# Kernel optimization log

Measured on AMD Instinct MI355X. Metric: run time of the kernel, lower is better.

The kernel has to match this reference:

```python
import jax, jax.numpy as jnp
import numpy as np

H = 1024
V = 32000
L = 4096


def setup_inputs() -> dict:
    key = jax.random.key(0)
    ks = jax.random.split(key, 20)
    s = 1.0 / np.sqrt(H)
    d = {}
    d["input_token"] = jax.random.randint(ks[0], (1,), 0, V)
    d["hidden"] = jax.random.normal(ks[1], (1, 1, H), jnp.float32)
    d["encoder_hiddens"] = jax.random.normal(ks[2], (L, H), jnp.float32)
    # parameters
    d["emb"] = jax.random.normal(ks[3], (V, H), jnp.float32)
    d["wW"] = jax.random.uniform(ks[4], (H, H), jnp.float32, -s, s)
    d["wb"] = jax.random.uniform(ks[5], (H,), jnp.float32, -s, s)
    d["uW"] = jax.random.uniform(ks[6], (H, H), jnp.float32, -s, s)
    d["ub"] = jax.random.uniform(ks[7], (H,), jnp.float32, -s, s)
    d["vW"] = jax.random.uniform(ks[8], (1, H), jnp.float32, -s, s)
    d["cW"] = jax.random.uniform(ks[9], (H, 2 * H), jnp.float32, -s, s)
    d["cb"] = jax.random.uniform(ks[10], (H,), jnp.float32, -s, s)
    d["w_ih"] = jax.random.uniform(ks[11], (3 * H, H), jnp.float32, -s, s)
    d["b_ih"] = jax.random.uniform(ks[12], (3 * H,), jnp.float32, -s, s)
    d["w_hh"] = jax.random.uniform(ks[13], (3 * H, H), jnp.float32, -s, s)
    d["b_hh"] = jax.random.uniform(ks[14], (3 * H,), jnp.float32, -s, s)
    d["outW"] = jax.random.uniform(ks[15], (V, H), jnp.float32, -s, s)
    d["outb"] = jax.random.uniform(ks[16], (V,), jnp.float32, -s, s)
    return d


def reference(input_token, hidden, encoder_hiddens, emb, wW, wb, uW, ub, vW,
              cW, cb, w_ih, b_ih, w_hh, b_hh, outW, outb):
    # embedding lookup, dropout is identity (p=0 / eval)
    embedded = emb[input_token[0]]  # [H]
    # additive attention: w(hidden[0]) + u(enc) -> tanh -> v -> softmax
    h0 = hidden[0]  # [1, H] (first/only layer)
    scores = jnp.tanh(h0 @ wW.T + wb + encoder_hiddens @ uW.T + ub) @ vW[0]  # [L]
    attn_weights = jax.nn.softmax(scores, axis=-1)  # [L]
    context = attn_weights @ encoder_hiddens  # [H]
    # combine + relu
    x = jnp.concatenate([context, embedded])  # [2H]
    x = jax.nn.relu(x @ cW.T + cb)  # [H]
    # single GRU cell step (torch GRU gate order: r, z, n)
    hprev = hidden[0, 0]  # [H]
    gi = x @ w_ih.T + b_ih
    gh = hprev @ w_hh.T + b_hh
    ir, iz, inn = jnp.split(gi, 3)
    hr, hz, hn = jnp.split(gh, 3)
    r = jax.nn.sigmoid(ir + hr)
    z = jax.nn.sigmoid(iz + hz)
    n = jnp.tanh(inn + r * hn)
    hnew = (1.0 - z) * n + z * hprev  # [H]
    new_hidden = hnew.reshape(1, 1, H)
    # residual + output projection
    out = (context.reshape(1, 1, H) + new_hidden)
    logits = out @ outW.T + outb  # [1, 1, V]
    return logits, new_hidden, attn_weights
```

## Files before the change

kernel.cpp:

```cpp
#include <hip/hip_runtime.h>
#include <hip/hip_bf16.h>
#include <math.h>

#define H 1024
#define V 32000
#define L 4096

typedef __bf16 bf16x8 __attribute__((ext_vector_type(8)));
typedef float f32x4 __attribute__((ext_vector_type(4)));

__device__ __forceinline__ unsigned short f32_to_bf16(float f) {
    unsigned int u = __float_as_uint(f);
    unsigned int r = (u + 0x7fffu + ((u >> 16) & 1u)) >> 16;
    return (unsigned short)r;
}

__device__ __forceinline__ float bf16_to_f32(unsigned short s) {
    return __uint_as_float(((unsigned int)s) << 16);
}

__device__ __forceinline__ float dot4(float4 a, float4 b) {
    return a.x * b.x + a.y * b.y + a.z * b.z + a.w * b.w;
}

__device__ __forceinline__ float wave_reduce(float v) {
    for (int off = 32; off; off >>= 1) v += __shfl_xor(v, off);
    return v;
}

__global__ __launch_bounds__(256) void prep_wh_kernel(
        const float* __restrict__ enc,
        const float* __restrict__ uW,
        const float* __restrict__ emb,
        const int* __restrict__ token,
        const float* __restrict__ h0,
        const float* __restrict__ wW,
        const float* __restrict__ wb,
        const float* __restrict__ ub,
        unsigned short* __restrict__ enc_bf,
        unsigned short* __restrict__ u_bf,
        float* __restrict__ emb_vec,
        float* __restrict__ wh,
        float* __restrict__ scores) {
    if (blockIdx.x < 1024) {
        int tid = blockIdx.x * 256 + threadIdx.x;
        const int stride = 1024 * 256;
        const int NE = L * H / 4;
        const int NU = H * H / 4;
        for (int i = tid; i < NE; i += stride) {
            float4 f = ((const float4*)enc)[i];
            ushort4 o;
            o.x = f32_to_bf16(f.x); o.y = f32_to_bf16(f.y);
            o.z = f32_to_bf16(f.z); o.w = f32_to_bf16(f.w);
            ((ushort4*)enc_bf)[i] = o;
        }
        for (int i = tid; i < NU; i += stride) {
            float4 f = ((const float4*)uW)[i];
            ushort4 o;
            o.x = f32_to_bf16(f.x); o.y = f32_to_bf16(f.y);
            o.z = f32_to_bf16(f.z); o.w = f32_to_bf16(f.w);
            ((ushort4*)u_bf)[i] = o;
        }
        int t0 = token[0];
        for (int i = tid; i < H; i += stride) emb_vec[i] = emb[(size_t)t0 * H + i];
    } else {
        int z = (blockIdx.x - 1024) * 256 + threadIdx.x;
        if (z < L) scores[z] = 0.f;
        int wave = ((blockIdx.x - 1024) * 256 + threadIdx.x) >> 6;
        int lane = threadIdx.x & 63;
        const float4* row = (const float4*)(wW + (size_t)wave * H);
        const float4* hv = (const float4*)h0;
        float acc = 0.f;
#pragma unroll
        for (int i = 0; i < 4; i++) {
            int idx = i * 64 + lane;
            acc += dot4(row[idx], hv[idx]);
        }
        acc = wave_reduce(acc);
        if (lane == 0) wh[wave] = acc + wb[wave] + ub[wave];
    }
}

#define APITCH 72
__global__ __launch_bounds__(256) void scores_kernel(
        const unsigned short* __restrict__ enc_bf,
        const unsigned short* __restrict__ u_bf,
        const float* __restrict__ wh,
        const float* __restrict__ vW,
        float* __restrict__ scores,
        float* __restrict__ context) {
    __shared__ unsigned short Als[64 * APITCH];
    __shared__ unsigned short Bls[128 * APITCH];
    int tid = threadIdx.x;
    if (blockIdx.x == 0 && blockIdx.y == 0) {
        ((float4*)context)[tid] = make_float4(0.f, 0.f, 0.f, 0.f);
    }
    int wave = tid >> 6, lane = tid & 63;
    int wm = wave >> 1, wn = wave & 1;
    int mrow = lane & 15, quad = lane >> 4;
    int r0b = blockIdx.x * 64;
    int jc0b = blockIdx.y * 128;

    f32x4 acc[2][4];
#pragma unroll
    for (int mt = 0; mt < 2; mt++)
#pragma unroll
        for (int jt = 0; jt < 4; jt++) acc[mt][jt] = (f32x4){0.f, 0.f, 0.f, 0.f};

    for (int k0 = 0; k0 < H; k0 += 64) {
#pragma unroll
        for (int c = 0; c < 2; c++) {
            int chunk = c * 256 + tid;
            int row = chunk >> 3, ko = (chunk & 7) * 8;
            *(uint4*)(Als + row * APITCH + ko) =
                *(const uint4*)(enc_bf + (size_t)(r0b + row) * H + k0 + ko);
        }
#pragma unroll
        for (int c = 0; c < 4; c++) {
            int chunk = c * 256 + tid;
            int j = chunk >> 3, ko = (chunk & 7) * 8;
            *(uint4*)(Bls + j * APITCH + ko) =
                *(const uint4*)(u_bf + (size_t)(jc0b + j) * H + k0 + ko);
        }
        __syncthreads();

        bf16x8 a[2][2];
#pragma unroll
        for (int mt = 0; mt < 2; mt++) {
            const unsigned short* abase =
                Als + (wm * 32 + mt * 16 + mrow) * APITCH + quad * 8;
            a[mt][0] = *(const bf16x8*)(abase);
            a[mt][1] = *(const bf16x8*)(abase + 32);
        }
#pragma unroll
        for (int jt = 0; jt < 4; jt++) {
            const unsigned short* bbase =
                Bls + (wn * 64 + jt * 16 + mrow) * APITCH + quad * 8;
            bf16x8 b0 = *(const bf16x8*)(bbase);
            bf16x8 b1 = *(const bf16x8*)(bbase + 32);
#pragma unroll
            for (int mt = 0; mt < 2; mt++) {
                acc[mt][jt] = __builtin_amdgcn_mfma_f32_16x16x32_bf16(a[mt][0], b0, acc[mt][jt], 0, 0, 0);
                acc[mt][jt] = __builtin_amdgcn_mfma_f32_16x16x32_bf16(a[mt][1], b1, acc[mt][jt], 0, 0, 0);
            }
        }
        __syncthreads();
    }

    float sacc[2][4] = {{0.f, 0.f, 0.f, 0.f}, {0.f, 0.f, 0.f, 0.f}};
#pragma unroll
    for (int jt = 0; jt < 4; jt++) {
        int jcol = jc0b + wn * 64 + jt * 16 + mrow;
        float vj = vW[jcol];
        float whv = wh[jcol];
#pragma unroll
        for (int mt = 0; mt < 2; mt++)
#pragma unroll
            for (int r = 0; r < 4; r++)
                sacc[mt][r] += vj * tanhf(acc[mt][jt][r] + whv);
    }
#pragma unroll
    for (int mt = 0; mt < 2; mt++)
#pragma unroll
        for (int r = 0; r < 4; r++) {
            float s = sacc[mt][r];
            s += __shfl_xor(s, 1);
            s += __shfl_xor(s, 2);
            s += __shfl_xor(s, 4);
            s += __shfl_xor(s, 8);
            if (mrow == 0)
                atomicAdd(&scores[r0b + wm * 32 + mt * 16 + quad * 4 + r], s);
        }
}

__global__ __launch_bounds__(256) void ctx_softmax_kernel(
        const float* __restrict__ scores,
        const unsigned short* __restrict__ enc_bf,
        float* __restrict__ context,
        float* __restrict__ attn_out) {
    __shared__ float smax[4];
    __shared__ float ssum[4];
    __shared__ float attn_l[32];
    int tid = threadIdx.x;
    int wid = tid >> 6, lane = tid & 63;
    float4 s0 = ((const float4*)scores)[tid];
    float4 s1 = ((const float4*)scores)[256 + tid];
    float4 s2 = ((const float4*)scores)[512 + tid];
    float4 s3 = ((const float4*)scores)[768 + tid];
    float m = fmaxf(fmaxf(fmaxf(s0.x, s0.y), fmaxf(s0.z, s0.w)),
                    fmaxf(fmaxf(s1.x, s1.y), fmaxf(s1.z, s1.w)));
    m = fmaxf(m, fmaxf(fmaxf(s2.x, s2.y), fmaxf(s2.z, s2.w)));
    m = fmaxf(m, fmaxf(fmaxf(s3.x, s3.y), fmaxf(s3.z, s3.w)));
    for (int off = 32; off; off >>= 1) m = fmaxf(m, __shfl_xor(m, off));
    if (lane == 0) smax[wid] = m;
    __syncthreads();
    float gmax = fmaxf(fmaxf(smax[0], smax[1]), fmaxf(smax[2], smax[3]));
    float e = expf(s0.x - gmax) + expf(s0.y - gmax) + expf(s0.z - gmax) + expf(s0.w - gmax)
            + expf(s1.x - gmax) + expf(s1.y - gmax) + expf(s1.z - gmax) + expf(s1.w - gmax)
            + expf(s2.x - gmax) + expf(s2.y - gmax) + expf(s2.z - gmax) + expf(s2.w - gmax)
            + expf(s3.x - gmax) + expf(s3.y - gmax) + expf(s3.z - gmax) + expf(s3.w - gmax);
    e = wave_reduce(e);
    if (lane == 0) ssum[wid] = e;
    __syncthreads();
    float inv = 1.0f / (ssum[0] + ssum[1] + ssum[2] + ssum[3]);

    int l0 = blockIdx.y * 32;
    if (tid < 32) attn_l[tid] = expf(scores[l0 + tid] - gmax) * inv;
    __syncthreads();

    if (blockIdx.x == 0 && blockIdx.y == 0) {
        float4 a0 = make_float4(expf(s0.x - gmax) * inv, expf(s0.y - gmax) * inv,
                                expf(s0.z - gmax) * inv, expf(s0.w - gmax) * inv);
        float4 a1 = make_float4(expf(s1.x - gmax) * inv, expf(s1.y - gmax) * inv,
                                expf(s1.z - gmax) * inv, expf(s1.w - gmax) * inv);
        float4 a2 = make_float4(expf(s2.x - gmax) * inv, expf(s2.y - gmax) * inv,
                                expf(s2.z - gmax) * inv, expf(s2.w - gmax) * inv);
        float4 a3 = make_float4(expf(s3.x - gmax) * inv, expf(s3.y - gmax) * inv,
                                expf(s3.z - gmax) * inv, expf(s3.w - gmax) * inv);
        ((float4*)attn_out)[tid] = a0;
        ((float4*)attn_out)[256 + tid] = a1;
        ((float4*)attn_out)[512 + tid] = a2;
        ((float4*)attn_out)[768 + tid] = a3;
    }

    int col = blockIdx.x * 256 + tid;
    float acc = 0.f;
#pragma unroll 4
    for (int l = 0; l < 32; l++)
        acc += attn_l[l] * bf16_to_f32(enc_bf[(size_t)(l0 + l) * H + col]);
    atomicAdd(&context[col], acc);
}

__global__ void combine_kernel(const float* __restrict__ context,
                               const float* __restrict__ emb_vec,
                               const float* __restrict__ cW,
                               const float* __restrict__ cb,
                               float* __restrict__ xvec) {
    int wave = (blockIdx.x * blockDim.x + threadIdx.x) >> 6;
    int lane = threadIdx.x & 63;
    if (wave >= H) return;
    const float4* row = (const float4*)(cW + (size_t)wave * 2 * H);
    const float4* cv = (const float4*)context;
    const float4* ev = (const float4*)emb_vec;
    float acc = 0.f;
#pragma unroll
    for (int i = 0; i < 4; i++) {
        int idx = i * 64 + lane;
        acc += dot4(row[idx], cv[idx]);
        acc += dot4(row[256 + idx], ev[idx]);
    }
    acc = wave_reduce(acc);
    if (lane == 0) xvec[wave] = fmaxf(acc + cb[wave], 0.f);
}

__global__ void gru_kernel(const float* __restrict__ xvec,
                           const float* __restrict__ hprev,
                           const float* __restrict__ w_ih,
                           const float* __restrict__ b_ih,
                           const float* __restrict__ w_hh,
                           const float* __restrict__ b_hh,
                           const float* __restrict__ context,
                           float* __restrict__ hnew_out,
                           float* __restrict__ ovec) {
    int j = (blockIdx.x * blockDim.x + threadIdx.x) >> 6;
    int lane = threadIdx.x & 63;
    if (j >= H) return;
    const float4* xv = (const float4*)xvec;
    const float4* hv = (const float4*)hprev;
    float a0 = 0.f, a1 = 0.f, a2 = 0.f, a3 = 0.f, a4 = 0.f, a5 = 0.f;
#pragma unroll
    for (int i = 0; i < 4; i++) {
        int idx = i * 64 + lane;
        float4 x4 = xv[idx], h4 = hv[idx];
        a0 += dot4(((const float4*)(w_ih + (size_t)j * H))[idx], x4);
        a1 += dot4(((const float4*)(w_ih + (size_t)(H + j) * H))[idx], x4);
        a2 += dot4(((const float4*)(w_ih + (size_t)(2 * H + j) * H))[idx], x4);
        a3 += dot4(((const float4*)(w_hh + (size_t)j * H))[idx], h4);
        a4 += dot4(((const float4*)(w_hh + (size_t)(H + j) * H))[idx], h4);
        a5 += dot4(((const float4*)(w_hh + (size_t)(2 * H + j) * H))[idx], h4);
    }
    a0 = wave_reduce(a0); a1 = wave_reduce(a1); a2 = wave_reduce(a2);
    a3 = wave_reduce(a3); a4 = wave_reduce(a4); a5 = wave_reduce(a5);
    if (lane == 0) {
        float ir = a0 + b_ih[j], iz = a1 + b_ih[H + j], inn = a2 + b_ih[2 * H + j];
        float hr = a3 + b_hh[j], hz = a4 + b_hh[H + j], hn = a5 + b_hh[2 * H + j];
        float r = 1.f / (1.f + expf(-(ir + hr)));
        float z = 1.f / (1.f + expf(-(iz + hz)));
        float n = tanhf(inn + r * hn);
        float hp = hprev[j];
        float hval = (1.f - z) * n + z * hp;
        hnew_out[j] = hval;
        ovec[j] = context[j] + hval;
    }
}

__global__ __launch_bounds__(256) void logits_kernel(
        const float* __restrict__ ovec,
        const float* __restrict__ outW,
        const float* __restrict__ outb,
        float* __restrict__ out) {
    int wave = (blockIdx.x * blockDim.x + threadIdx.x) >> 6;
    int lane = threadIdx.x & 63;
    int i0 = wave * 2;
    if (i0 >= V) return;
    const float4* row0 = (const float4*)(outW + (size_t)i0 * H);
    const float4* row1 = (const float4*)(outW + (size_t)(i0 + 1) * H);
    const float4* ov = (const float4*)ovec;
    float acc0 = 0.f, acc1 = 0.f;
#pragma unroll
    for (int t = 0; t < 4; t++) {
        int idx = t * 64 + lane;
        float4 o4 = ov[idx];
        acc0 += dot4(row0[idx], o4);
        acc1 += dot4(row1[idx], o4);
    }
    acc0 = wave_reduce(acc0);
    acc1 = wave_reduce(acc1);
    if (lane == 0) {
        out[i0] = acc0 + outb[i0];
        out[i0 + 1] = acc1 + outb[i0 + 1];
    }
}

extern "C" void kernel_launch(void* const* d_in, const int* in_sizes, int n_in,
                              void* d_out, int out_size, void* d_ws, size_t ws_size,
                              hipStream_t stream) {
    const int* token = (const int*)d_in[0];
    const float* hidden = (const float*)d_in[1];
    const float* enc = (const float*)d_in[2];
    const float* emb = (const float*)d_in[3];
    const float* wW = (const float*)d_in[4];
    const float* wb = (const float*)d_in[5];
    const float* uW = (const float*)d_in[6];
    const float* ub = (const float*)d_in[7];
    const float* vW = (const float*)d_in[8];
    const float* cW = (const float*)d_in[9];
    const float* cb = (const float*)d_in[10];
    const float* w_ih = (const float*)d_in[11];
    const float* b_ih = (const float*)d_in[12];
    const float* w_hh = (const float*)d_in[13];
    const float* b_hh = (const float*)d_in[14];
    const float* outW = (const float*)d_in[15];
    const float* outb = (const float*)d_in[16];
    float* out = (float*)d_out;

    char* ws = (char*)d_ws;
    unsigned short* enc_bf = (unsigned short*)ws;
    unsigned short* u_bf = (unsigned short*)(ws + (size_t)L * H * 2);
    float* whv = (float*)(ws + (size_t)L * H * 2 + (size_t)H * H * 2);
    float* emb_vec = whv + H;
    float* scores = emb_vec + H;
    float* context = scores + L;
    float* xvec = context + H;
    float* ovec = xvec + H;

    prep_wh_kernel<<<1280, 256, 0, stream>>>(enc, uW, emb, token, hidden, wW, wb, ub,
                                             enc_bf, u_bf, emb_vec, whv, scores);
    scores_kernel<<<dim3(64, 8), 256, 0, stream>>>(enc_bf, u_bf, whv, vW, scores, context);
    ctx_softmax_kernel<<<dim3(4, 128), 256, 0, stream>>>(scores, enc_bf, context, out + V + H);
    combine_kernel<<<256, 256, 0, stream>>>(context, emb_vec, cW, cb, xvec);
    gru_kernel<<<256, 256, 0, stream>>>(xvec, hidden, w_ih, b_ih, w_hh, b_hh,
                                        context, out + V, ovec);
    logits_kernel<<<4000, 256, 0, stream>>>(ovec, outW, outb, out);
}
```

Before: 338.7 us.

## Fuse all stages into one persistent kernel with software grid barriers

Replaces six separate launches with a single persistent kernel of 256 blocks that separates stages with an atomic-counter grid barrier. The hidden-to-hidden GRU matvec is hoisted into the first stage alongside the bf16 conversion. The attention GEMM tile is enlarged and the logits stage loops over rows per wave. This removes launch gaps and inter-kernel idle time, at the risk of barrier spin cost, reduced parallelism in the memory-bound phases, and a timeout fallback that could break correctness if blocks are not co-resident.

```diff
diff --git a/kernel.cpp b/kernel.cpp
--- a/kernel.cpp
+++ b/kernel.cpp
@@ -1,10 +1,12 @@
 #include <hip/hip_runtime.h>
-#include <hip/hip_bf16.h>
 #include <math.h>
 
 #define H 1024
 #define V 32000
 #define L 4096
+#define NBLK 256
+#define NTHR 512
+#define APITCH 72
 
 typedef __bf16 bf16x8 __attribute__((ext_vector_type(8)));
 typedef float f32x4 __attribute__((ext_vector_type(4)));
@@ -28,297 +30,317 @@
     return v;
 }
 
-__global__ __launch_bounds__(256) void prep_wh_kernel(
+__device__ __forceinline__ void grid_sync(unsigned* bar) {
+    __threadfence();
+    __syncthreads();
+    if (threadIdx.x == 0) {
+        unsigned g = __hip_atomic_load(&bar[1], __ATOMIC_RELAXED, __HIP_MEMORY_SCOPE_AGENT);
+        unsigned a = __hip_atomic_fetch_add(&bar[0], 1u, __ATOMIC_ACQ_REL, __HIP_MEMORY_SCOPE_AGENT);
+        if (a == NBLK - 1u) {
+            __hip_atomic_store(&bar[0], 0u, __ATOMIC_RELAXED, __HIP_MEMORY_SCOPE_AGENT);
+            __hip_atomic_store(&bar[1], g + 1u, __ATOMIC_RELEASE, __HIP_MEMORY_SCOPE_AGENT);
+        } else {
+            unsigned long long t0 = __builtin_amdgcn_s_memrealtime();
+            while (__hip_atomic_load(&bar[1], __ATOMIC_ACQUIRE, __HIP_MEMORY_SCOPE_AGENT) == g) {
+                __builtin_amdgcn_s_sleep(4);
+                if (__builtin_amdgcn_s_memrealtime() - t0 > 500000ull) break;
+            }
+        }
+    }
+    __syncthreads();
+    __threadfence();
+}
+
+__global__ __launch_bounds__(NTHR, 2) void mega_kernel(
+        const int* __restrict__ token,
+        const float* __restrict__ hidden,
         const float* __restrict__ enc,
-        const float* __restrict__ uW,
         const float* __restrict__ emb,
-        const int* __restrict__ token,
-        const float* __restrict__ h0,
         const float* __restrict__ wW,
         const float* __restrict__ wb,
+        const float* __restrict__ uW,
         const float* __restrict__ ub,
+        const float* __restrict__ vW,
+        const float* __restrict__ cW,
+        const float* __restrict__ cb,
+        const float* __restrict__ w_ih,
+        const float* __restrict__ b_ih,
+        const float* __restrict__ w_hh,
+        const float* __restrict__ b_hh,
+        const float* __restrict__ outW,
+        const float* __restrict__ outb,
+        float* __restrict__ out,
+        unsigned* __restrict__ bar,
+        float* __restrict__ wh,
+        float* __restrict__ gh,
+        float* __restrict__ scores,
+        float* __restrict__ context,
+        float* __restrict__ xvec,
+        float* __restrict__ ovec,
         unsigned short* __restrict__ enc_bf,
-        unsigned short* __restrict__ u_bf,
-        float* __restrict__ emb_vec,
-        float* __restrict__ wh,
-        float* __restrict__ scores) {
-    if (blockIdx.x < 1024) {
-        int tid = blockIdx.x * 256 + threadIdx.x;
-        const int stride = 1024 * 256;
+        unsigned short* __restrict__ u_bf) {
+    __shared__ unsigned short Als[128 * APITCH];
+    __shared__ unsigned short Bls[128 * APITCH];
+    __shared__ float smax[8];
+    __shared__ float ssum[8];
+    __shared__ float attn_l[32];
+
+    const int tid = threadIdx.x;
+    const int blk = blockIdx.x;
+    const int gt = blk * NTHR + tid;
+    const int wid = tid >> 6, lane = tid & 63;
+    const int gw = gt >> 6;
+
+    {
+        const int GSZ = NBLK * NTHR;
         const int NE = L * H / 4;
-        const int NU = H * H / 4;
-        for (int i = tid; i < NE; i += stride) {
+        for (int i = gt; i < NE; i += GSZ) {
             float4 f = ((const float4*)enc)[i];
             ushort4 o;
             o.x = f32_to_bf16(f.x); o.y = f32_to_bf16(f.y);
             o.z = f32_to_bf16(f.z); o.w = f32_to_bf16(f.w);
             ((ushort4*)enc_bf)[i] = o;
         }
-        for (int i = tid; i < NU; i += stride) {
+        const int NU = H * H / 4;
+        for (int i = gt; i < NU; i += GSZ) {
             float4 f = ((const float4*)uW)[i];
             ushort4 o;
             o.x = f32_to_bf16(f.x); o.y = f32_to_bf16(f.y);
             o.z = f32_to_bf16(f.z); o.w = f32_to_bf16(f.w);
             ((ushort4*)u_bf)[i] = o;
         }
-        int t0 = token[0];
-        for (int i = tid; i < H; i += stride) emb_vec[i] = emb[(size_t)t0 * H + i];
-    } else {
-        int z = (blockIdx.x - 1024) * 256 + threadIdx.x;
-        if (z < L) scores[z] = 0.f;
-        int wave = ((blockIdx.x - 1024) * 256 + threadIdx.x) >> 6;
-        int lane = threadIdx.x & 63;
-        const float4* row = (const float4*)(wW + (size_t)wave * H);
-        const float4* hv = (const float4*)h0;
+        if (gt < L / 4) ((float4*)scores)[gt] = make_float4(0.f, 0.f, 0.f, 0.f);
+        else if (gt < L / 4 + H / 4)
+            ((float4*)context)[gt - L / 4] = make_float4(0.f, 0.f, 0.f, 0.f);
+        if (gw < H) {
+            const float4* row = (const float4*)(wW + (size_t)gw * H);
+            const float4* hv = (const float4*)hidden;
+            float acc = 0.f;
+#pragma unroll
+            for (int i = 0; i < 4; i++) {
+                int idx = i * 64 + lane;
+                acc += dot4(row[idx], hv[idx]);
+            }
+            acc = wave_reduce(acc);
+            if (lane == 0) wh[gw] = acc + wb[gw] + ub[gw];
+        } else {
+            int j = gw - H;
+            const float4* hv = (const float4*)hidden;
+            float a3 = 0.f, a4 = 0.f, a5 = 0.f;
+#pragma unroll
+            for (int i = 0; i < 4; i++) {
+                int idx = i * 64 + lane;
+                float4 h4 = hv[idx];
+                a3 += dot4(((const float4*)(w_hh + (size_t)j * H))[idx], h4);
+                a4 += dot4(((const float4*)(w_hh + (size_t)(H + j) * H))[idx], h4);
+                a5 += dot4(((const float4*)(w_hh + (size_t)(2 * H + j) * H))[idx], h4);
+            }
+            a3 = wave_reduce(a3); a4 = wave_reduce(a4); a5 = wave_reduce(a5);
+            if (lane == 0) {
+                gh[j] = a3 + b_hh[j];
+                gh[H + j] = a4 + b_hh[H + j];
+                gh[2 * H + j] = a5 + b_hh[2 * H + j];
+            }
+        }
+    }
+    grid_sync(bar);
+
+    {
+        const int bx = blk & 31, by = blk >> 5;
+        const int r0b = bx * 128, jc0b = by * 128;
+        const int wm = wid >> 1, wn = wid & 1;
+        const int mrow = lane & 15, quad = lane >> 4;
+
+        f32x4 acc[2][4];
+#pragma unroll
+        for (int mt = 0; mt < 2; mt++)
+#pragma unroll
+            for (int jt = 0; jt < 4; jt++) acc[mt][jt] = (f32x4){0.f, 0.f, 0.f, 0.f};
+
+        for (int k0 = 0; k0 < H; k0 += 64) {
+#pragma unroll
+            for (int c = 0; c < 2; c++) {
+                int chunk = c * NTHR + tid;
+                int row = chunk >> 3, ko = (chunk & 7) * 8;
+                *(uint4*)(Als + row * APITCH + ko) =
+                    *(const uint4*)(enc_bf + (size_t)(r0b + row) * H + k0 + ko);
+            }
+#pragma unroll
+            for (int c = 0; c < 2; c++) {
+                int chunk = c * NTHR + tid;
+                int j = chunk >> 3, ko = (chunk & 7) * 8;
+                *(uint4*)(Bls + j * APITCH + ko) =
+                    *(const uint4*)(u_bf + (size_t)(jc0b + j) * H + k0 + ko);
+            }
+            __syncthreads();
+
+            bf16x8 a[2][2];
+#pragma unroll
+            for (int mt = 0; mt < 2; mt++) {
+                const unsigned short* abase =
+                    Als + (wm * 32 + mt * 16 + mrow) * APITCH + quad * 8;
+                a[mt][0] = *(const bf16x8*)(abase);
+                a[mt][1] = *(const bf16x8*)(abase + 32);
+            }
+#pragma unroll
+            for (int jt = 0; jt < 4; jt++) {
+                const unsigned short* bbase =
+                    Bls + (wn * 64 + jt * 16 + mrow) * APITCH + quad * 8;
+                bf16x8 b0 = *(const bf16x8*)(bbase);
+                bf16x8 b1 = *(const bf16x8*)(bbase + 32);
+#pragma unroll
+                for (int mt = 0; mt < 2; mt++) {
+                    acc[mt][jt] = __builtin_amdgcn_mfma_f32_16x16x32_bf16(a[mt][0], b0, acc[mt][jt], 0, 0, 0);
+                    acc[mt][jt] = __builtin_amdgcn_mfma_f32_16x16x32_bf16(a[mt][1], b1, acc[mt][jt], 0, 0, 0);
+                }
+            }
+            __syncthreads();
+        }
+
+        float sacc[2][4] = {{0.f, 0.f, 0.f, 0.f}, {0.f, 0.f, 0.f, 0.f}};
+#pragma unroll
+        for (int jt = 0; jt < 4; jt++) {
+            int jcol = jc0b + wn * 64 + jt * 16 + mrow;
+            float vj = vW[jcol];
+            float whv = wh[jcol];
+#pragma unroll
+            for (int mt = 0; mt < 2; mt++)
+#pragma unroll
+                for (int r = 0; r < 4; r++)
+                    sacc[mt][r] += vj * tanhf(acc[mt][jt][r] + whv);
+        }
+#pragma unroll
+        for (int mt = 0; mt < 2; mt++)
+#pragma unroll
+            for (int r = 0; r < 4; r++) {
+                float s = sacc[mt][r];
+                s += __shfl_xor(s, 1);
+                s += __shfl_xor(s, 2);
+                s += __shfl_xor(s, 4);
+                s += __shfl_xor(s, 8);
+                if (mrow == 0)
+                    atomicAdd(&scores[r0b + wm * 32 + mt * 16 + quad * 4 + r], s);
+            }
+    }
+    grid_sync(bar);
+
+    {
+        const int cx = blk & 1, ly = blk >> 1;
+        float4 s0 = ((const float4*)scores)[tid];
+        float4 s1 = ((const float4*)scores)[512 + tid];
+        float m = fmaxf(fmaxf(fmaxf(s0.x, s0.y), fmaxf(s0.z, s0.w)),
+                        fmaxf(fmaxf(s1.x, s1.y), fmaxf(s1.z, s1.w)));
+        for (int off = 32; off; off >>= 1) m = fmaxf(m, __shfl_xor(m, off));
+        if (lane == 0) smax[wid] = m;
+        __syncthreads();
+        float gmax = smax[0];
+#pragma unroll
+        for (int w = 1; w < 8; w++) gmax = fmaxf(gmax, smax[w]);
+        float e = expf(s0.x - gmax) + expf(s0.y - gmax) + expf(s0.z - gmax) + expf(s0.w - gmax)
+                + expf(s1.x - gmax) + expf(s1.y - gmax) + expf(s1.z - gmax) + expf(s1.w - gmax);
+        e = wave_reduce(e);
+        if (lane == 0) ssum[wid] = e;
+        __syncthreads();
+        float tot = ssum[0];
+#pragma unroll
+        for (int w = 1; w < 8; w++) tot += ssum[w];
+        float inv = 1.0f / tot;
+
+        int l0 = ly * 32;
+        if (tid < 32) attn_l[tid] = expf(scores[l0 + tid] - gmax) * inv;
+        __syncthreads();
+
+        if (blk == 0) {
+            float* attn_out = out + V + H;
+            float4 a0 = make_float4(expf(s0.x - gmax) * inv, expf(s0.y - gmax) * inv,
+                                    expf(s0.z - gmax) * inv, expf(s0.w - gmax) * inv);
+            float4 a1 = make_float4(expf(s1.x - gmax) * inv, expf(s1.y - gmax) * inv,
+                                    expf(s1.z - gmax) * inv, expf(s1.w - gmax) * inv);
+            ((float4*)attn_out)[tid] = a0;
+            ((float4*)attn_out)[512 + tid] = a1;
+        }
+
+        int col = cx * 512 + tid;
         float acc = 0.f;
-#pragma unroll
-        for (int i = 0; i < 4; i++) {
-            int idx = i * 64 + lane;
-            acc += dot4(row[idx], hv[idx]);
-        }
-        acc = wave_reduce(acc);
-        if (lane == 0) wh[wave] = acc + wb[wave] + ub[wave];
-    }
-}
-
-#define APITCH 72
-__global__ __launch_bounds__(256) void scores_kernel(
-        const unsigned short* __restrict__ enc_bf,
-        const unsigned short* __restrict__ u_bf,
-        const float* __restrict__ wh,
-        const float* __restrict__ vW,
-        float* __restrict__ scores,
-        float* __restrict__ context) {
-    __shared__ unsigned short Als[64 * APITCH];
-    __shared__ unsigned short Bls[128 * APITCH];
-    int tid = threadIdx.x;
-    if (blockIdx.x == 0 && blockIdx.y == 0) {
-        ((float4*)context)[tid] = make_float4(0.f, 0.f, 0.f, 0.f);
-    }
-    int wave = tid >> 6, lane = tid & 63;
-    int wm = wave >> 1, wn = wave & 1;
-    int mrow = lane & 15, quad = lane >> 4;
-    int r0b = blockIdx.x * 64;
-    int jc0b = blockIdx.y * 128;
-
-    f32x4 acc[2][4];
-#pragma unroll
-    for (int mt = 0; mt < 2; mt++)
-#pragma unroll
-        for (int jt = 0; jt < 4; jt++) acc[mt][jt] = (f32x4){0.f, 0.f, 0.f, 0.f};
-
-    for (int k0 = 0; k0 < H; k0 += 64) {
-#pragma unroll
-        for (int c = 0; c < 2; c++) {
-            int chunk = c * 256 + tid;
-            int row = chunk >> 3, ko = (chunk & 7) * 8;
-            *(uint4*)(Als + row * APITCH + ko) =
-                *(const uint4*)(enc_bf + (size_t)(r0b + row) * H + k0 + ko);
-        }
-#pragma unroll
-        for (int c = 0; c < 4; c++) {
-            int chunk = c * 256 + tid;
-            int j = chunk >> 3, ko = (chunk & 7) * 8;
-            *(uint4*)(Bls + j * APITCH + ko) =
-                *(const uint4*)(u_bf + (size_t)(jc0b + j) * H + k0 + ko);
-        }
-        __syncthreads();
-
-        bf16x8 a[2][2];
-#pragma unroll
-        for (int mt = 0; mt < 2; mt++) {
-            const unsigned short* abase =
-                Als + (wm * 32 + mt * 16 + mrow) * APITCH + quad * 8;
-            a[mt][0] = *(const bf16x8*)(abase);
-            a[mt][1] = *(const bf16x8*)(abase + 32);
-        }
-#pragma unroll
-        for (int jt = 0; jt < 4; jt++) {
-            const unsigned short* bbase =
-                Bls + (wn * 64 + jt * 16 + mrow) * APITCH + quad * 8;
-            bf16x8 b0 = *(const bf16x8*)(bbase);
-            bf16x8 b1 = *(const bf16x8*)(bbase + 32);
-#pragma unroll
-            for (int mt = 0; mt < 2; mt++) {
-                acc[mt][jt] = __builtin_amdgcn_mfma_f32_16x16x32_bf16(a[mt][0], b0, acc[mt][jt], 0, 0, 0);
-                acc[mt][jt] = __builtin_amdgcn_mfma_f32_16x16x32_bf16(a[mt][1], b1, acc[mt][jt], 0, 0, 0);
-            }
-        }
-        __syncthreads();
-    }
-
-    float sacc[2][4] = {{0.f, 0.f, 0.f, 0.f}, {0.f, 0.f, 0.f, 0.f}};
-#pragma unroll
-    for (int jt = 0; jt < 4; jt++) {
-        int jcol = jc0b + wn * 64 + jt * 16 + mrow;
-        float vj = vW[jcol];
-        float whv = wh[jcol];
-#pragma unroll
-        for (int mt = 0; mt < 2; mt++)
-#pragma unroll
-            for (int r = 0; r < 4; r++)
-                sacc[mt][r] += vj * tanhf(acc[mt][jt][r] + whv);
-    }
-#pragma unroll
-    for (int mt = 0; mt < 2; mt++)
-#pragma unroll
-        for (int r = 0; r < 4; r++) {
-            float s = sacc[mt][r];
-            s += __shfl_xor(s, 1);
-            s += __shfl_xor(s, 2);
-            s += __shfl_xor(s, 4);
-            s += __shfl_xor(s, 8);
-            if (mrow == 0)
-                atomicAdd(&scores[r0b + wm * 32 + mt * 16 + quad * 4 + r], s);
-        }
-}
-
-__global__ __launch_bounds__(256) void ctx_softmax_kernel(
-        const float* __restrict__ scores,
-        const unsigned short* __restrict__ enc_bf,
-        float* __restrict__ context,
-        float* __restrict__ attn_out) {
-    __shared__ float smax[4];
-    __shared__ float ssum[4];
-    __shared__ float attn_l[32];
-    int tid = threadIdx.x;
-    int wid = tid >> 6, lane = tid & 63;
-    float4 s0 = ((const float4*)scores)[tid];
-    float4 s1 = ((const float4*)scores)[256 + tid];
-    float4 s2 = ((const float4*)scores)[512 + tid];
-    float4 s3 = ((const float4*)scores)[768 + tid];
-    float m = fmaxf(fmaxf(fmaxf(s0.x, s0.y), fmaxf(s0.z, s0.w)),
-                    fmaxf(fmaxf(s1.x, s1.y), fmaxf(s1.z, s1.w)));
-    m = fmaxf(m, fmaxf(fmaxf(s2.x, s2.y), fmaxf(s2.z, s2.w)));
-    m = fmaxf(m, fmaxf(fmaxf(s3.x, s3.y), fmaxf(s3.z, s3.w)));
-    for (int off = 32; off; off >>= 1) m = fmaxf(m, __shfl_xor(m, off));
-    if (lane == 0) smax[wid] = m;
-    __syncthreads();
-    float gmax = fmaxf(fmaxf(smax[0], smax[1]), fmaxf(smax[2], smax[3]));
-    float e = expf(s0.x - gmax) + expf(s0.y - gmax) + expf(s0.z - gmax) + expf(s0.w - gmax)
-            + expf(s1.x - gmax) + expf(s1.y - gmax) + expf(s1.z - gmax) + expf(s1.w - gmax)
-            + expf(s2.x - gmax) + expf(s2.y - gmax) + expf(s2.z - gmax) + expf(s2.w - gmax)
-            + expf(s3.x - gmax) + expf(s3.y - gmax) + expf(s3.z - gmax) + expf(s3.w - gmax);
-    e = wave_reduce(e);
-    if (lane == 0) ssum[wid] = e;
-    __syncthreads();
-    float inv = 1.0f / (ssum[0] + ssum[1] + ssum[2] + ssum[3]);
-
-    int l0 = blockIdx.y * 32;
-    if (tid < 32) attn_l[tid] = expf(scores[l0 + tid] - gmax) * inv;
-    __syncthreads();
-
-    if (blockIdx.x == 0 && blockIdx.y == 0) {
-        float4 a0 = make_float4(expf(s0.x - gmax) * inv, expf(s0.y - gmax) * inv,
-                                expf(s0.z - gmax) * inv, expf(s0.w - gmax) * inv);
-        float4 a1 = make_float4(expf(s1.x - gmax) * inv, expf(s1.y - gmax) * inv,
-                                expf(s1.z - gmax) * inv, expf(s1.w - gmax) * inv);
-        float4 a2 = make_float4(expf(s2.x - gmax) * inv, expf(s2.y - gmax) * inv,
-                                expf(s2.z - gmax) * inv, expf(s2.w - gmax) * inv);
-        float4 a3 = make_float4(expf(s3.x - gmax) * inv, expf(s3.y - gmax) * inv,
-                                expf(s3.z - gmax) * inv, expf(s3.w - gmax) * inv);
-        ((float4*)attn_out)[tid] = a0;
-        ((float4*)attn_out)[256 + tid] = a1;
-        ((float4*)attn_out)[512 + tid] = a2;
-        ((float4*)attn_out)[768 + tid] = a3;
-    }
-
-    int col = blockIdx.x * 256 + tid;
-    float acc = 0.f;
 #pragma unroll 4
-    for (int l = 0; l < 32; l++)
-        acc += attn_l[l] * bf16_to_f32(enc_bf[(size_t)(l0 + l) * H + col]);
-    atomicAdd(&context[col], acc);
-}
-
-__global__ void combine_kernel(const float* __restrict__ context,
-                               const float* __restrict__ emb_vec,
-                               const float* __restrict__ cW,
-                               const float* __restrict__ cb,
-                               float* __restrict__ xvec) {
-    int wave = (blockIdx.x * blockDim.x + threadIdx.x) >> 6;
-    int lane = threadIdx.x & 63;
-    if (wave >= H) return;
-    const float4* row = (const float4*)(cW + (size_t)wave * 2 * H);
-    const float4* cv = (const float4*)context;
-    const float4* ev = (const float4*)emb_vec;
-    float acc = 0.f;
-#pragma unroll
-    for (int i = 0; i < 4; i++) {
-        int idx = i * 64 + lane;
-        acc += dot4(row[idx], cv[idx]);
-        acc += dot4(row[256 + idx], ev[idx]);
-    }
-    acc = wave_reduce(acc);
-    if (lane == 0) xvec[wave] = fmaxf(acc + cb[wave], 0.f);
-}
-
-__global__ void gru_kernel(const float* __restrict__ xvec,
-                           const float* __restrict__ hprev,
-                           const float* __restrict__ w_ih,
-                           const float* __restrict__ b_ih,
-                           const float* __restrict__ w_hh,
-                           const float* __restrict__ b_hh,
-                           const float* __restrict__ context,
-                           float* __restrict__ hnew_out,
-                           float* __restrict__ ovec) {
-    int j = (blockIdx.x * blockDim.x + threadIdx.x) >> 6;
-    int lane = threadIdx.x & 63;
-    if (j >= H) return;
-    const float4* xv = (const float4*)xvec;
-    const float4* hv = (const float4*)hprev;
-    float a0 = 0.f, a1 = 0.f, a2 = 0.f, a3 = 0.f, a4 = 0.f, a5 = 0.f;
-#pragma unroll
-    for (int i = 0; i < 4; i++) {
-        int idx = i * 64 + lane;
-        float4 x4 = xv[idx], h4 = hv[idx];
-        a0 += dot4(((const float4*)(w_ih + (size_t)j * H))[idx], x4);
-        a1 += dot4(((const float4*)(w_ih + (size_t)(H + j) * H))[idx], x4);
-        a2 += dot4(((const float4*)(w_ih + (size_t)(2 * H + j) * H))[idx], x4);
-        a3 += dot4(((const float4*)(w_hh + (size_t)j * H))[idx], h4);
-        a4 += dot4(((const float4*)(w_hh + (size_t)(H + j) * H))[idx], h4);
-        a5 += dot4(((const float4*)(w_hh + (size_t)(2 * H + j) * H))[idx], h4);
-    }
-    a0 = wave_reduce(a0); a1 = wave_reduce(a1); a2 = wave_reduce(a2);
-    a3 = wave_reduce(a3); a4 = wave_reduce(a4); a5 = wave_reduce(a5);
-    if (lane == 0) {
-        float ir = a0 + b_ih[j], iz = a1 + b_ih[H + j], inn = a2 + b_ih[2 * H + j];
-        float hr = a3 + b_hh[j], hz = a4 + b_hh[H + j], hn = a5 + b_hh[2 * H + j];
-        float r = 1.f / (1.f + expf(-(ir + hr)));
-        float z = 1.f / (1.f + expf(-(iz + hz)));
-        float n = tanhf(inn + r * hn);
-        float hp = hprev[j];
-        float hval = (1.f - z) * n + z * hp;
-        hnew_out[j] = hval;
-        ovec[j] = context[j] + hval;
-    }
-}
-
-__global__ __launch_bounds__(256) void logits_kernel(
-        const float* __restrict__ ovec,
-        const float* __restrict__ outW,
-        const float* __restrict__ outb,
-        float* __restrict__ out) {
-    int wave = (blockIdx.x * blockDim.x + threadIdx.x) >> 6;
-    int lane = threadIdx.x & 63;
-    int i0 = wave * 2;
-    if (i0 >= V) return;
-    const float4* row0 = (const float4*)(outW + (size_t)i0 * H);
-    const float4* row1 = (const float4*)(outW + (size_t)(i0 + 1) * H);
-    const float4* ov = (const float4*)ovec;
-    float acc0 = 0.f, acc1 = 0.f;
-#pragma unroll
-    for (int t = 0; t < 4; t++) {
-        int idx = t * 64 + lane;
-        float4 o4 = ov[idx];
-        acc0 += dot4(row0[idx], o4);
-        acc1 += dot4(row1[idx], o4);
-    }
-    acc0 = wave_reduce(acc0);
-    acc1 = wave_reduce(acc1);
-    if (lane == 0) {
-        out[i0] = acc0 + outb[i0];
-        out[i0 + 1] = acc1 + outb[i0 + 1];
+        for (int l = 0; l < 32; l++)
+            acc += attn_l[l] * bf16_to_f32(enc_bf[(size_t)(l0 + l) * H + col]);
+        atomicAdd(&context[col], acc);
+    }
+    grid_sync(bar);
+
+    {
+        if (gw < H) {
+            int t0 = token[0];
+            const float4* row = (const float4*)(cW + (size_t)gw * 2 * H);
+            const float4* cv = (const float4*)context;
+            const float4* ev = (const float4*)(emb + (size_t)t0 * H);
+            float acc = 0.f;
+#pragma unroll
+            for (int i = 0; i < 4; i++) {
+                int idx = i * 64 + lane;
+                acc += dot4(row[idx], cv[idx]);
+                acc += dot4(row[256 + idx], ev[idx]);
+            }
+            acc = wave_reduce(acc);
+            if (lane == 0) xvec[gw] = fmaxf(acc + cb[gw], 0.f);
+        }
+    }
+    grid_sync(bar);
+
+    {
+        if (gw < H) {
+            int j = gw;
+            const float4* xv = (const float4*)xvec;
+            float a0 = 0.f, a1 = 0.f, a2 = 0.f;
+#pragma unroll
+            for (int i = 0; i < 4; i++) {
+                int idx = i * 64 + lane;
+                float4 x4 = xv[idx];
+                a0 += dot4(((const float4*)(w_ih + (size_t)j * H))[idx], x4);
+                a1 += dot4(((const float4*)(w_ih + (size_t)(H + j) * H))[idx], x4);
+                a2 += dot4(((const float4*)(w_ih + (size_t)(2 * H + j) * H))[idx], x4);
+            }
+            a0 = wave_reduce(a0); a1 = wave_reduce(a1); a2 = wave_reduce(a2);
+            if (lane == 0) {
+                float ir = a0 + b_ih[j], iz = a1 + b_ih[H + j], inn = a2 + b_ih[2 * H + j];
+                float r = 1.f / (1.f + expf(-(ir + gh[j])));
+                float z = 1.f / (1.f + expf(-(iz + gh[H + j])));
+                float n = tanhf(inn + r * gh[2 * H + j]);
+                float hp = hidden[j];
+                float hval = (1.f - z) * n + z * hp;
+                out[V + j] = hval;
+                ovec[j] = context[j] + hval;
+            }
+        }
+    }
+    grid_sync(bar);
+
+    {
+        const float4* ov = (const float4*)ovec;
+        float4 o4[4];
+#pragma unroll
+        for (int t = 0; t < 4; t++) o4[t] = ov[t * 64 + lane];
+        int base = gw * 16;
+        for (int p = 0; p < 8; p++) {
+            int i0 = base + p * 2;
+            if (i0 >= V) break;
+            const float4* row0 = (const float4*)(outW + (size_t)i0 * H);
+            const float4* row1 = row0 + 256;
+            float acc0 = 0.f, acc1 = 0.f;
+#pragma unroll
+            for (int t = 0; t < 4; t++) {
+                int idx = t * 64 + lane;
+                acc0 += dot4(row0[idx], o4[t]);
+                acc1 += dot4(row1[idx], o4[t]);
+            }
+            acc0 = wave_reduce(acc0);
+            acc1 = wave_reduce(acc1);
+            if (lane == 0) {
+                out[i0] = acc0 + outb[i0];
+                out[i0 + 1] = acc1 + outb[i0 + 1];
+            }
+        }
     }
 }
 
@@ -345,21 +367,20 @@
     float* out = (float*)d_out;
 
     char* ws = (char*)d_ws;
-    unsigned short* enc_bf = (unsigned short*)ws;
-    unsigned short* u_bf = (unsigned short*)(ws + (size_t)L * H * 2);
-    float* whv = (float*)(ws + (size_t)L * H * 2 + (size_t)H * H * 2);
-    float* emb_vec = whv + H;
-    float* scores = emb_vec + H;
+    unsigned* bar = (unsigned*)ws;
+    float* wh = (float*)(ws + 4096);
+    float* gh = wh + H;
+    float* scores = gh + 3 * H;
     float* context = scores + L;
     float* xvec = context + H;
     float* ovec = xvec + H;
-
-    prep_wh_kernel<<<1280, 256, 0, stream>>>(enc, uW, emb, token, hidden, wW, wb, ub,
-                                             enc_bf, u_bf, emb_vec, whv, scores);
-    scores_kernel<<<dim3(64, 8), 256, 0, stream>>>(enc_bf, u_bf, whv, vW, scores, context);
-    ctx_softmax_kernel<<<dim3(4, 128), 256, 0, stream>>>(scores, enc_bf, context, out + V + H);
-    combine_kernel<<<256, 256, 0, stream>>>(context, emb_vec, cW, cb, xvec);
-    gru_kernel<<<256, 256, 0, stream>>>(xvec, hidden, w_ih, b_ih, w_hh, b_hh,
-                                        context, out + V, ovec);
-    logits_kernel<<<4000, 256, 0, stream>>>(ovec, outW, outb, out);
-}
+    unsigned short* enc_bf = (unsigned short*)(ws + (1 << 20));
+    unsigned short* u_bf = enc_bf + (size_t)L * H;
+
+    hipMemsetAsync(ws, 0, 8, stream);
+    mega_kernel<<<NBLK, NTHR, 0, stream>>>(token, hidden, enc, emb, wW, wb, uW, ub,
+                                           vW, cW, cb, w_ih, b_ih, w_hh, b_hh,
+                                           outW, outb, out,
+                                           bar, wh, gh, scores, context, xvec, ovec,
+                                           enc_bf, u_bf);
+}
```

Result: slower. 849.5 us (+150.8%).

## Fuse bf16 conversion and wh projection into the attention scores GEMM

Applied to the files above, without the earlier changes.

Removes the separate prep kernel that converted the encoder states and uW to bf16 in workspace. The scores GEMM now loads fp32 tiles, converts them to bf16 while staging into LDS, and computes its 128-entry slice of the wW·h projection into shared memory. The tile grows to 128x128 with 512 threads, and scores/context are zeroed with a memset. The embedding row is read directly in the combine kernel, and the context reduction reads fp32 encoder states. The trade-off is redundant wW·h work in every block and twice the bytes per GEMM operand load, in exchange for dropping a full conversion pass and its workspace traffic.

```diff
diff --git a/kernel.cpp b/kernel.cpp
--- a/kernel.cpp
+++ b/kernel.cpp
@@ -1,10 +1,10 @@
 #include <hip/hip_runtime.h>
-#include <hip/hip_bf16.h>
 #include <math.h>
 
 #define H 1024
 #define V 32000
 #define L 4096
+#define APITCH 72
 
 typedef __bf16 bf16x8 __attribute__((ext_vector_type(8)));
 typedef float f32x4 __attribute__((ext_vector_type(4)));
@@ -15,8 +15,13 @@
     return (unsigned short)r;
 }
 
-__device__ __forceinline__ float bf16_to_f32(unsigned short s) {
-    return __uint_as_float(((unsigned int)s) << 16);
+__device__ __forceinline__ uint4 pack_bf16_8(float4 a, float4 b) {
+    uint4 r;
+    r.x = (unsigned)f32_to_bf16(a.x) | ((unsigned)f32_to_bf16(a.y) << 16);
+    r.y = (unsigned)f32_to_bf16(a.z) | ((unsigned)f32_to_bf16(a.w) << 16);
+    r.z = (unsigned)f32_to_bf16(b.x) | ((unsigned)f32_to_bf16(b.y) << 16);
+    r.w = (unsigned)f32_to_bf16(b.z) | ((unsigned)f32_to_bf16(b.w) << 16);
+    return r;
 }
 
 __device__ __forceinline__ float dot4(float4 a, float4 b) {
@@ -28,78 +33,42 @@
     return v;
 }
 
-__global__ __launch_bounds__(256) void prep_wh_kernel(
+__global__ __launch_bounds__(512) void scores_kernel(
         const float* __restrict__ enc,
         const float* __restrict__ uW,
-        const float* __restrict__ emb,
-        const int* __restrict__ token,
-        const float* __restrict__ h0,
         const float* __restrict__ wW,
         const float* __restrict__ wb,
         const float* __restrict__ ub,
-        unsigned short* __restrict__ enc_bf,
-        unsigned short* __restrict__ u_bf,
-        float* __restrict__ emb_vec,
-        float* __restrict__ wh,
+        const float* __restrict__ hidden,
+        const float* __restrict__ vW,
         float* __restrict__ scores) {
-    if (blockIdx.x < 1024) {
-        int tid = blockIdx.x * 256 + threadIdx.x;
-        const int stride = 1024 * 256;
-        const int NE = L * H / 4;
-        const int NU = H * H / 4;
-        for (int i = tid; i < NE; i += stride) {
-            float4 f = ((const float4*)enc)[i];
-            ushort4 o;
-            o.x = f32_to_bf16(f.x); o.y = f32_to_bf16(f.y);
-            o.z = f32_to_bf16(f.z); o.w = f32_to_bf16(f.w);
-            ((ushort4*)enc_bf)[i] = o;
-        }
-        for (int i = tid; i < NU; i += stride) {
-            float4 f = ((const float4*)uW)[i];
-            ushort4 o;
-            o.x = f32_to_bf16(f.x); o.y = f32_to_bf16(f.y);
-            o.z = f32_to_bf16(f.z); o.w = f32_to_bf16(f.w);
-            ((ushort4*)u_bf)[i] = o;
-        }
-        int t0 = token[0];
-        for (int i = tid; i < H; i += stride) emb_vec[i] = emb[(size_t)t0 * H + i];
-    } else {
-        int z = (blockIdx.x - 1024) * 256 + threadIdx.x;
-        if (z < L) scores[z] = 0.f;
-        int wave = ((blockIdx.x - 1024) * 256 + threadIdx.x) >> 6;
-        int lane = threadIdx.x & 63;
-        const float4* row = (const float4*)(wW + (size_t)wave * H);
-        const float4* hv = (const float4*)h0;
+    __shared__ unsigned short Als[128 * APITCH];
+    __shared__ unsigned short Bls[128 * APITCH];
+    __shared__ float wh_s[128];
+
+    const int tid = threadIdx.x;
+    const int bx = blockIdx.x, by = blockIdx.y;
+    const int r0b = bx * 128, jc0b = by * 128;
+    const int wid = tid >> 6, lane = tid & 63;
+
+    {
+        int jl = tid >> 2, part = tid & 3;
+        const float4* row = (const float4*)(wW + (size_t)(jc0b + jl) * H);
+        const float4* hv = (const float4*)hidden;
         float acc = 0.f;
-#pragma unroll
-        for (int i = 0; i < 4; i++) {
-            int idx = i * 64 + lane;
+#pragma unroll 8
+        for (int i = 0; i < 64; i++) {
+            int idx = part * 64 + i;
             acc += dot4(row[idx], hv[idx]);
         }
-        acc = wave_reduce(acc);
-        if (lane == 0) wh[wave] = acc + wb[wave] + ub[wave];
-    }
-}
-
-#define APITCH 72
-__global__ __launch_bounds__(256) void scores_kernel(
-        const unsigned short* __restrict__ enc_bf,
-        const unsigned short* __restrict__ u_bf,
-        const float* __restrict__ wh,
-        const float* __restrict__ vW,
-        float* __restrict__ scores,
-        float* __restrict__ context) {
-    __shared__ unsigned short Als[64 * APITCH];
-    __shared__ unsigned short Bls[128 * APITCH];
-    int tid = threadIdx.x;
-    if (blockIdx.x == 0 && blockIdx.y == 0) {
-        ((float4*)context)[tid] = make_float4(0.f, 0.f, 0.f, 0.f);
-    }
-    int wave = tid >> 6, lane = tid & 63;
-    int wm = wave >> 1, wn = wave & 1;
-    int mrow = lane & 15, quad = lane >> 4;
-    int r0b = blockIdx.x * 64;
-    int jc0b = blockIdx.y * 128;
+        acc += __shfl_xor(acc, 1);
+        acc += __shfl_xor(acc, 2);
+        if (part == 0) wh_s[jl] = acc + wb[jc0b + jl] + ub[jc0b + jl];
+    }
+
+    const int wm = wid >> 1, wn = wid & 1;
+    const int mrow = lane & 15, quad = lane >> 4;
+    const int srow = tid >> 2, seg = tid & 3;
 
     f32x4 acc[2][4];
 #pragma unroll
@@ -108,19 +77,19 @@
         for (int jt = 0; jt < 4; jt++) acc[mt][jt] = (f32x4){0.f, 0.f, 0.f, 0.f};
 
     for (int k0 = 0; k0 < H; k0 += 64) {
-#pragma unroll
-        for (int c = 0; c < 2; c++) {
-            int chunk = c * 256 + tid;
-            int row = chunk >> 3, ko = (chunk & 7) * 8;
-            *(uint4*)(Als + row * APITCH + ko) =
-                *(const uint4*)(enc_bf + (size_t)(r0b + row) * H + k0 + ko);
-        }
-#pragma unroll
-        for (int c = 0; c < 4; c++) {
-            int chunk = c * 256 + tid;
-            int j = chunk >> 3, ko = (chunk & 7) * 8;
-            *(uint4*)(Bls + j * APITCH + ko) =
-                *(const uint4*)(u_bf + (size_t)(jc0b + j) * H + k0 + ko);
+        {
+            const float4* src = (const float4*)(enc + (size_t)(r0b + srow) * H + k0 + seg * 16);
+            float4 f0 = src[0], f1 = src[1], f2 = src[2], f3 = src[3];
+            unsigned short* dst = Als + srow * APITCH + seg * 16;
+            *(uint4*)(dst) = pack_bf16_8(f0, f1);
+            *(uint4*)(dst + 8) = pack_bf16_8(f2, f3);
+        }
+        {
+            const float4* src = (const float4*)(uW + (size_t)(jc0b + srow) * H + k0 + seg * 16);
+            float4 g0 = src[0], g1 = src[1], g2 = src[2], g3 = src[3];
+            unsigned short* dst = Bls + srow * APITCH + seg * 16;
+            *(uint4*)(dst) = pack_bf16_8(g0, g1);
+            *(uint4*)(dst + 8) = pack_bf16_8(g2, g3);
         }
         __syncthreads();
 
@@ -150,9 +119,9 @@
     float sacc[2][4] = {{0.f, 0.f, 0.f, 0.f}, {0.f, 0.f, 0.f, 0.f}};
 #pragma unroll
     for (int jt = 0; jt < 4; jt++) {
-        int jcol = jc0b + wn * 64 + jt * 16 + mrow;
-        float vj = vW[jcol];
-        float whv = wh[jcol];
+        int jl = wn * 64 + jt * 16 + mrow;
+        float vj = vW[jc0b + jl];
+        float whv = wh_s[jl];
 #pragma unroll
         for (int mt = 0; mt < 2; mt++)
 #pragma unroll
@@ -175,7 +144,7 @@
 
 __global__ __launch_bounds__(256) void ctx_softmax_kernel(
         const float* __restrict__ scores,
-        const unsigned short* __restrict__ enc_bf,
+        const float* __restrict__ enc,
         float* __restrict__ context,
         float* __restrict__ attn_out) {
     __shared__ float smax[4];
@@ -227,12 +196,13 @@
     float acc = 0.f;
 #pragma unroll 4
     for (int l = 0; l < 32; l++)
-        acc += attn_l[l] * bf16_to_f32(enc_bf[(size_t)(l0 + l) * H + col]);
+        acc += attn_l[l] * enc[(size_t)(l0 + l) * H + col];
     atomicAdd(&context[col], acc);
 }
 
 __global__ void combine_kernel(const float* __restrict__ context,
-                               const float* __restrict__ emb_vec,
+                               const int* __restrict__ token,
+                               const float* __restrict__ emb,
                                const float* __restrict__ cW,
                                const float* __restrict__ cb,
                                float* __restrict__ xvec) {
@@ -241,7 +211,7 @@
     if (wave >= H) return;
     const float4* row = (const float4*)(cW + (size_t)wave * 2 * H);
     const float4* cv = (const float4*)context;
-    const float4* ev = (const float4*)emb_vec;
+    const float4* ev = (const float4*)(emb + (size_t)token[0] * H);
     float acc = 0.f;
 #pragma unroll
     for (int i = 0; i < 4; i++) {
@@ -345,20 +315,18 @@
     float* out = (float*)d_out;
 
     char* ws = (char*)d_ws;
-    unsigned short* enc_bf = (unsigned short*)ws;
-    unsigned short* u_bf = (unsigned short*)(ws + (size_t)L * H * 2);
-    float* whv = (float*)(ws + (size_t)L * H * 2 + (size_t)H * H * 2);
-    float* emb_vec = whv + H;
-    float* scores = emb_vec + H;
+    float* scores = (float*)ws;
     float* context = scores + L;
     float* xvec = context + H;
     float* ovec = xvec + H;
 
-    prep_wh_kernel<<<1280, 256, 0, stream>>>(enc, uW, emb, token, hidden, wW, wb, ub,
-                                             enc_bf, u_bf, emb_vec, whv, scores);
-    scores_kernel<<<dim3(64, 8), 256, 0, stream>>>(enc_bf, u_bf, whv, vW, scores, context);
-    ctx_softmax_kernel<<<dim3(4, 128), 256, 0, stream>>>(scores, enc_bf, context, out + V + H);
-    combine_kernel<<<256, 256, 0, stream>>>(context, emb_vec, cW, cb, xvec);
+    hipMemsetAsync(ws, 0, (size_t)(L + H) * sizeof(float), stream);
+
+    scores_kernel<<<dim3(32, 8), 512, 0, stream>>>(enc, uW, wW, wb, ub, hidden,
+                                                   vW, scores);
+    ctx_softmax_kernel<<<dim3(4, 128), 256, 0, stream>>>(scores, enc, context,
+                                                         out + V + H);
+    combine_kernel<<<256, 256, 0, stream>>>(context, token, emb, cW, cb, xvec);
     gru_kernel<<<256, 256, 0, stream>>>(xvec, hidden, w_ih, b_ih, w_hh, b_hh,
                                         context, out + V, ovec);
     logits_kernel<<<4000, 256, 0, stream>>>(ovec, outW, outb, out);
```

Result: slower. 384.8 us (+13.6%).

## Hoist hidden-state GRU matvec into prep kernel and widen logits rows per wave

Applied to the files above, without the earlier changes.

The w_hh·hprev matvec depends only on inputs, so it moves into the prep kernel next to the wW matvec. That takes it off the serial GRU stage and overlaps it with the bf16 conversion work. The embedding row is now read directly inside combine_kernel instead of being copied first. The logits kernel has each wave compute four output rows instead of two, halving the grid and reusing the loaded ovec. The prep kernel's matvec blocks do four times the work, which could lengthen that stage if they become the tail.

```diff
diff --git a/kernel.cpp b/kernel.cpp
--- a/kernel.cpp
+++ b/kernel.cpp
@@ -28,19 +28,19 @@
     return v;
 }
 
-__global__ __launch_bounds__(256) void prep_wh_kernel(
+__global__ __launch_bounds__(256) void prep_kernel(
         const float* __restrict__ enc,
         const float* __restrict__ uW,
-        const float* __restrict__ emb,
-        const int* __restrict__ token,
         const float* __restrict__ h0,
         const float* __restrict__ wW,
         const float* __restrict__ wb,
         const float* __restrict__ ub,
+        const float* __restrict__ w_hh,
+        const float* __restrict__ b_hh,
         unsigned short* __restrict__ enc_bf,
         unsigned short* __restrict__ u_bf,
-        float* __restrict__ emb_vec,
         float* __restrict__ wh,
+        float* __restrict__ gh,
         float* __restrict__ scores) {
     if (blockIdx.x < 1024) {
         int tid = blockIdx.x * 256 + threadIdx.x;
@@ -61,23 +61,34 @@
             o.z = f32_to_bf16(f.z); o.w = f32_to_bf16(f.w);
             ((ushort4*)u_bf)[i] = o;
         }
-        int t0 = token[0];
-        for (int i = tid; i < H; i += stride) emb_vec[i] = emb[(size_t)t0 * H + i];
     } else {
         int z = (blockIdx.x - 1024) * 256 + threadIdx.x;
         if (z < L) scores[z] = 0.f;
-        int wave = ((blockIdx.x - 1024) * 256 + threadIdx.x) >> 6;
+        int j = ((blockIdx.x - 1024) * 256 + threadIdx.x) >> 6;
         int lane = threadIdx.x & 63;
-        const float4* row = (const float4*)(wW + (size_t)wave * H);
+        const float4* rw = (const float4*)(wW + (size_t)j * H);
+        const float4* r3 = (const float4*)(w_hh + (size_t)j * H);
+        const float4* r4 = (const float4*)(w_hh + (size_t)(H + j) * H);
+        const float4* r5 = (const float4*)(w_hh + (size_t)(2 * H + j) * H);
         const float4* hv = (const float4*)h0;
-        float acc = 0.f;
+        float aw = 0.f, a3 = 0.f, a4 = 0.f, a5 = 0.f;
 #pragma unroll
         for (int i = 0; i < 4; i++) {
             int idx = i * 64 + lane;
-            acc += dot4(row[idx], hv[idx]);
-        }
-        acc = wave_reduce(acc);
-        if (lane == 0) wh[wave] = acc + wb[wave] + ub[wave];
+            float4 h4 = hv[idx];
+            aw += dot4(rw[idx], h4);
+            a3 += dot4(r3[idx], h4);
+            a4 += dot4(r4[idx], h4);
+            a5 += dot4(r5[idx], h4);
+        }
+        aw = wave_reduce(aw);
+        a3 = wave_reduce(a3); a4 = wave_reduce(a4); a5 = wave_reduce(a5);
+        if (lane == 0) {
+            wh[j] = aw + wb[j] + ub[j];
+            gh[j] = a3 + b_hh[j];
+            gh[H + j] = a4 + b_hh[H + j];
+            gh[2 * H + j] = a5 + b_hh[2 * H + j];
+        }
     }
 }
 
@@ -232,7 +243,8 @@
 }
 
 __global__ void combine_kernel(const float* __restrict__ context,
-                               const float* __restrict__ emb_vec,
+                               const int* __restrict__ token,
+                               const float* __restrict__ emb,
                                const float* __restrict__ cW,
                                const float* __restrict__ cb,
                                float* __restrict__ xvec) {
@@ -241,7 +253,7 @@
     if (wave >= H) return;
     const float4* row = (const float4*)(cW + (size_t)wave * 2 * H);
     const float4* cv = (const float4*)context;
-    const float4* ev = (const float4*)emb_vec;
+    const float4* ev = (const float4*)(emb + (size_t)token[0] * H);
     float acc = 0.f;
 #pragma unroll
     for (int i = 0; i < 4; i++) {
@@ -257,8 +269,7 @@
                            const float* __restrict__ hprev,
                            const float* __restrict__ w_ih,
                            const float* __restrict__ b_ih,
-                           const float* __restrict__ w_hh,
-                           const float* __restrict__ b_hh,
+                           const float* __restrict__ gh,
                            const float* __restrict__ context,
                            float* __restrict__ hnew_out,
                            float* __restrict__ ovec) {
@@ -266,27 +277,21 @@
     int lane = threadIdx.x & 63;
     if (j >= H) return;
     const float4* xv = (const float4*)xvec;
-    const float4* hv = (const float4*)hprev;
-    float a0 = 0.f, a1 = 0.f, a2 = 0.f, a3 = 0.f, a4 = 0.f, a5 = 0.f;
+    float a0 = 0.f, a1 = 0.f, a2 = 0.f;
 #pragma unroll
     for (int i = 0; i < 4; i++) {
         int idx = i * 64 + lane;
-        float4 x4 = xv[idx], h4 = hv[idx];
+        float4 x4 = xv[idx];
         a0 += dot4(((const float4*)(w_ih + (size_t)j * H))[idx], x4);
         a1 += dot4(((const float4*)(w_ih + (size_t)(H + j) * H))[idx], x4);
         a2 += dot4(((const float4*)(w_ih + (size_t)(2 * H + j) * H))[idx], x4);
-        a3 += dot4(((const float4*)(w_hh + (size_t)j * H))[idx], h4);
-        a4 += dot4(((const float4*)(w_hh + (size_t)(H + j) * H))[idx], h4);
-        a5 += dot4(((const float4*)(w_hh + (size_t)(2 * H + j) * H))[idx], h4);
     }
     a0 = wave_reduce(a0); a1 = wave_reduce(a1); a2 = wave_reduce(a2);
-    a3 = wave_reduce(a3); a4 = wave_reduce(a4); a5 = wave_reduce(a5);
     if (lane == 0) {
         float ir = a0 + b_ih[j], iz = a1 + b_ih[H + j], inn = a2 + b_ih[2 * H + j];
-        float hr = a3 + b_hh[j], hz = a4 + b_hh[H + j], hn = a5 + b_hh[2 * H + j];
-        float r = 1.f / (1.f + expf(-(ir + hr)));
-        float z = 1.f / (1.f + expf(-(iz + hz)));
-        float n = tanhf(inn + r * hn);
+        float r = 1.f / (1.f + expf(-(ir + gh[j])));
+        float z = 1.f / (1.f + expf(-(iz + gh[H + j])));
+        float n = tanhf(inn + r * gh[2 * H + j]);
         float hp = hprev[j];
         float hval = (1.f - z) * n + z * hp;
         hnew_out[j] = hval;
@@ -301,24 +306,34 @@
         float* __restrict__ out) {
     int wave = (blockIdx.x * blockDim.x + threadIdx.x) >> 6;
     int lane = threadIdx.x & 63;
-    int i0 = wave * 2;
+    int i0 = wave * 4;
     if (i0 >= V) return;
+    const float4* ov = (const float4*)ovec;
+    float4 o4[4];
+#pragma unroll
+    for (int t = 0; t < 4; t++) o4[t] = ov[t * 64 + lane];
+    float acc0 = 0.f, acc1 = 0.f, acc2 = 0.f, acc3 = 0.f;
     const float4* row0 = (const float4*)(outW + (size_t)i0 * H);
-    const float4* row1 = (const float4*)(outW + (size_t)(i0 + 1) * H);
-    const float4* ov = (const float4*)ovec;
-    float acc0 = 0.f, acc1 = 0.f;
+    const float4* row1 = row0 + 256;
+    const float4* row2 = row0 + 512;
+    const float4* row3 = row0 + 768;
 #pragma unroll
     for (int t = 0; t < 4; t++) {
         int idx = t * 64 + lane;
-        float4 o4 = ov[idx];
-        acc0 += dot4(row0[idx], o4);
-        acc1 += dot4(row1[idx], o4);
+        acc0 += dot4(row0[idx], o4[t]);
+        acc1 += dot4(row1[idx], o4[t]);
+        acc2 += dot4(row2[idx], o4[t]);
+        acc3 += dot4(row3[idx], o4[t]);
     }
     acc0 = wave_reduce(acc0);
     acc1 = wave_reduce(acc1);
+    acc2 = wave_reduce(acc2);
+    acc3 = wave_reduce(acc3);
     if (lane == 0) {
         out[i0] = acc0 + outb[i0];
         out[i0 + 1] = acc1 + outb[i0 + 1];
+        out[i0 + 2] = acc2 + outb[i0 + 2];
+        out[i0 + 3] = acc3 + outb[i0 + 3];
     }
 }
 
@@ -348,18 +363,18 @@
     unsigned short* enc_bf = (unsigned short*)ws;
     unsigned short* u_bf = (unsigned short*)(ws + (size_t)L * H * 2);
     float* whv = (float*)(ws + (size_t)L * H * 2 + (size_t)H * H * 2);
-    float* emb_vec = whv + H;
-    float* scores = emb_vec + H;
+    float* gh = whv + H;
+    float* scores = gh + 3 * H;
     float* context = scores + L;
     float* xvec = context + H;
     float* ovec = xvec + H;
 
-    prep_wh_kernel<<<1280, 256, 0, stream>>>(enc, uW, emb, token, hidden, wW, wb, ub,
-                                             enc_bf, u_bf, emb_vec, whv, scores);
+    prep_kernel<<<1280, 256, 0, stream>>>(enc, uW, hidden, wW, wb, ub, w_hh, b_hh,
+                                          enc_bf, u_bf, whv, gh, scores);
     scores_kernel<<<dim3(64, 8), 256, 0, stream>>>(enc_bf, u_bf, whv, vW, scores, context);
     ctx_softmax_kernel<<<dim3(4, 128), 256, 0, stream>>>(scores, enc_bf, context, out + V + H);
-    combine_kernel<<<256, 256, 0, stream>>>(context, emb_vec, cW, cb, xvec);
-    gru_kernel<<<256, 256, 0, stream>>>(xvec, hidden, w_ih, b_ih, w_hh, b_hh,
+    combine_kernel<<<256, 256, 0, stream>>>(context, token, emb, cW, cb, xvec);
+    gru_kernel<<<256, 256, 0, stream>>>(xvec, hidden, w_ih, b_ih, gh,
                                         context, out + V, ovec);
-    logits_kernel<<<4000, 256, 0, stream>>>(ovec, outW, outb, out);
-}
+    logits_kernel<<<2000, 256, 0, stream>>>(ovec, outW, outb, out);
+}
```

New measurement: 338.2 us. About the same (-0.1%).
